# Optimization experiments

Hardware: AMD Instinct MI355X
Metric: run time of the kernel (lower is better)

The kernel has to match this reference:

```python
import jax, jax.numpy as jnp
import numpy as np

EMBED = 1024
HEADS = 16
HEAD_DIM = EMBED // HEADS


def setup_inputs() -> dict:
    key = jax.random.key(0)
    ks = jax.random.split(key, 6)
    N, S = 4, 1024
    query = jax.random.normal(ks[0], (N, S, EMBED), dtype=jnp.float32)
    keys = jax.random.normal(ks[1], (N, S, EMBED), dtype=jnp.float32)
    values = jax.random.normal(ks[2], (N, S, EMBED), dtype=jnp.float32)
    mask = jax.random.randint(ks[3], (N, 1, S, S), 0, 2, dtype=jnp.int32)
    W_out = jax.random.normal(ks[4], (EMBED, EMBED), dtype=jnp.float32) * (1.0 / np.sqrt(EMBED))
    b_out = jax.random.normal(ks[5], (EMBED,), dtype=jnp.float32) * 0.02
    return {"query": query, "keys": keys, "values": values, "mask": mask,
            "W_out": W_out, "b_out": b_out}


def reference(query, keys, values, mask, W_out, b_out):
    N, Q, _ = query.shape
    K = keys.shape[1]
    # NOTE: the torch module never applies its per-head q/k/v Linear layers;
    # only the reshape + attention + fc_out are in the forward path.
    q = query.reshape(N, Q, HEADS, HEAD_DIM)
    k = keys.reshape(N, K, HEADS, HEAD_DIM)
    v = values.reshape(N, K, HEADS, HEAD_DIM)
    # energy: [N, H, Q, K]
    energy = jnp.einsum("bqhd,bkhd->bhqk", q, k)
    energy = jnp.where(mask == 0, jnp.float32(-1e20), energy)
    attn = jax.nn.softmax(energy / jnp.sqrt(jnp.float32(HEAD_DIM)), axis=3)
    out = jnp.einsum("bhqk,bkhd->bqhd", attn, v).reshape(N, Q, HEADS * HEAD_DIM)
    return out @ W_out.T + b_out
```

## Files before the change

### kernel.cpp

```cpp
#include <hip/hip_runtime.h>
#include <math.h>

#define NB 4
#define SL 1024
#define EMB 1024
#define NH 16
#define HD 64
#define QB 64

typedef __attribute__((ext_vector_type(8))) short bf16x8;
typedef __attribute__((ext_vector_type(4))) float f32x4;
typedef __attribute__((ext_vector_type(4))) unsigned u32x4;

static __device__ __forceinline__ unsigned pk2(float a, float b) {
    unsigned x = __float_as_uint(a) + 0x8000u;
    unsigned y = __float_as_uint(b) + 0x8000u;
    return (x >> 16) | (y & 0xFFFF0000u);
}
static __device__ __forceinline__ float exp2_fast(float x) {
    float r; asm("v_exp_f32 %0, %1" : "=v"(r) : "v"(x)); return r;
}
static __device__ __forceinline__ void gload_lds16(const void* g, void* l) {
    __builtin_amdgcn_global_load_lds(
        (const __attribute__((address_space(1))) unsigned int*)g,
        (__attribute__((address_space(3))) unsigned int*)l, 16, 0, 0);
}

#define VMW(n) asm volatile("s_waitcnt vmcnt(" #n ")" ::: "memory")
#define MEMPIN() asm volatile("" ::: "memory")

__global__ __launch_bounds__(256) void prep(
    const float* __restrict__ W, unsigned short* __restrict__ Wb,
    const float* __restrict__ Kf, unsigned short* __restrict__ Kb,
    const float* __restrict__ V, unsigned short* __restrict__ Vt,
    const int* __restrict__ mask, unsigned long long* __restrict__ Mbt)
{
    __shared__ unsigned short sT[128 * 68];
    const int bid = blockIdx.x, tid = threadIdx.x;

    if (bid < 512) {
        int i = (bid * 256 + tid) * 8;
        float4 f0 = *(const float4*)&W[i];
        float4 f1 = *(const float4*)&W[i + 4];
        uint4 u = { pk2(f0.x,f0.y), pk2(f0.z,f0.w), pk2(f1.x,f1.y), pk2(f1.z,f1.w) };
        *(uint4*)&Wb[i] = u;
    } else if (bid < 2560) {
        int t = bid - 512;
        int b = t >> 9, h = (t >> 5) & 15, k0 = (t & 31) * 32;
        int r = tid >> 3, d = (tid & 7) * 8;
        const float* gp = &Kf[((size_t)(b * SL + k0 + r)) * EMB + h * HD + d];
        float4 f0 = *(const float4*)gp, f1 = *(const float4*)(gp + 4);
        uint4 u = { pk2(f0.x,f0.y), pk2(f0.z,f0.w), pk2(f1.x,f1.y), pk2(f1.z,f1.w) };
        *(uint4*)&Kb[((size_t)((b * NH + h) * SL + k0 + r)) * HD + d] = u;
    } else if (bid < 3072) {
        int t = bid - 2560;
        int bh = t >> 3, kb = t & 7;
        int b = bh >> 4, h = bh & 15;
        int k0 = kb * 128;
        #pragma unroll
        for (int i = 0; i < 4; ++i) {
            int lin = (i * 256 + tid) * 8;
            int r = lin >> 6, d = lin & 63;
            const float* gp = &V[((size_t)(b * SL + k0 + r)) * EMB + h * HD + d];
            float4 f0 = *(const float4*)gp, f1 = *(const float4*)(gp + 4);
            uint2 u0 = { pk2(f0.x,f0.y), pk2(f0.z,f0.w) };
            uint2 u1 = { pk2(f1.x,f1.y), pk2(f1.z,f1.w) };
            *(uint2*)&sT[r * 68 + d]     = u0;
            *(uint2*)&sT[r * 68 + d + 4] = u1;
        }
        __syncthreads();
        #pragma unroll
        for (int p = 0; p < 4; ++p) {
            int d = p * 16 + (tid >> 4);
            int c = tid & 15;
            unsigned v[4];
            #pragma unroll
            for (int j = 0; j < 4; ++j) {
                unsigned lo = sT[(c * 8 + 2 * j) * 68 + d];
                unsigned hi = sT[(c * 8 + 2 * j + 1) * 68 + d];
                v[j] = lo | (hi << 16);
            }
            uint4 u = { v[0], v[1], v[2], v[3] };
            *(uint4*)&Vt[((size_t)(bh * HD + d)) * SL + k0 + c * 8] = u;
        }
    } else {
        int t = bid - 3072;
        int lane = tid & 63;
        #pragma unroll
        for (int r = 0; r < 4; ++r) {
            int wid = (t * 4 + (tid >> 6)) * 4 + r;
            int c = wid & 15, q = (wid >> 4) & 1023, bb = wid >> 14;
            int mv = mask[((size_t)bb * SL + q) * SL + c * 64 + lane];
            unsigned long long bits = __ballot(mv != 0);
            if (lane == 0) Mbt[((size_t)bb * 16 + c) * SL + q] = bits;
        }
    }
}

__global__ __launch_bounds__(256, 3) void attn_mfma(
    const float* __restrict__ Q, const unsigned short* __restrict__ Kb,
    const unsigned short* __restrict__ Vt,
    const unsigned long long* __restrict__ Mbt,
    unsigned short* __restrict__ Oa)
{
    const int lin = blockIdx.x;
    const int xcd = lin & 7, slot = lin >> 3;
    const int bh = xcd * 8 + (slot >> 4);
    const int q0 = (slot & 15) * QB;
    const int b = bh >> 4, h = bh & 15;
    const int tid = threadIdx.x;
    const int w = tid >> 6, lane = tid & 63;
    const int m16 = lane & 15, quad = lane >> 4;
    const int lr = lane >> 3, lc = lane & 7;

    __shared__ __align__(16) unsigned short sK[3][64 * 64];
    __shared__ __align__(16) unsigned short sVt[3][64 * 64];

    const size_t vbase = (size_t)(bh * HD) * SL;
    const size_t kbase = (size_t)(bh * SL) * HD;
    const size_t mbase = (size_t)(b * 16) * SL + q0 + w * 16 + m16;

    bf16x8 bQ[2];
    {
        const float* qp = &Q[((size_t)(b * SL + q0 + w * 16 + m16)) * EMB + h * HD + quad * 8];
        float4 f0 = *(const float4*)qp,        f1 = *(const float4*)(qp + 4);
        float4 f2 = *(const float4*)(qp + 32), f3 = *(const float4*)(qp + 36);
        u32x4 u0 = { pk2(f0.x,f0.y), pk2(f0.z,f0.w), pk2(f1.x,f1.y), pk2(f1.z,f1.w) };
        u32x4 u1 = { pk2(f2.x,f2.y), pk2(f2.z,f2.w), pk2(f3.x,f3.y), pk2(f3.z,f3.w) };
        bQ[0] = __builtin_bit_cast(bf16x8, u0);
        bQ[1] = __builtin_bit_cast(bf16x8, u1);
    }
    MEMPIN();
    unsigned long long mbA, mbB, mbC = 0;
    #pragma unroll
    for (int i = 0; i < 2; ++i) {
        int row = w * 16 + i * 8;
        gload_lds16(&Vt[vbase + (size_t)(row + lr) * SL + (lc ^ lr) * 8], &sVt[0][row * 64]);
        gload_lds16(&Kb[kbase + (size_t)(row + lr) * HD + (lc ^ lr) * 8], &sK[0][row * 64]);
    }
    MEMPIN();
    mbA = Mbt[mbase];
    MEMPIN();
    #pragma unroll
    for (int i = 0; i < 2; ++i) {
        int row = w * 16 + i * 8;
        gload_lds16(&Vt[vbase + (size_t)(row + lr) * SL + 64 + (lc ^ lr) * 8], &sVt[1][row * 64]);
        gload_lds16(&Kb[kbase + (size_t)(64 + row + lr) * HD + (lc ^ lr) * 8], &sK[1][row * 64]);
    }
    MEMPIN();
    mbB = Mbt[mbase + SL];
    MEMPIN();

    unsigned short* kc = (unsigned short*)sK[0];
    unsigned short* kn = (unsigned short*)sK[1];
    unsigned short* k2 = (unsigned short*)sK[2];
    unsigned short* vc = (unsigned short*)sVt[0];
    unsigned short* vn = (unsigned short*)sVt[1];
    unsigned short* v2 = (unsigned short*)sVt[2];

    f32x4 O[4] = {};
    f32x4 lacc = {};
    const float CSC = 0.125f * 1.44269504f;
    const short one_bf = (short)0x3F80;
    const bf16x8 ones = { one_bf, one_bf, one_bf, one_bf, one_bf, one_bf, one_bf, one_bf };

    for (int kt = 0; kt < 16; ++kt) {
        if (kt < 15) { VMW(5); } else { VMW(1); }
        __builtin_amdgcn_s_barrier();
        __builtin_amdgcn_sched_barrier(0);

        if (kt < 14) {
            const int k0n = (kt + 2) * 64;
            #pragma unroll
            for (int i = 0; i < 2; ++i) {
                int row = w * 16 + i * 8;
                gload_lds16(&Vt[vbase + (size_t)(row + lr) * SL + k0n + (lc ^ lr) * 8],
                            &v2[row * 64]);
                gload_lds16(&Kb[kbase + (size_t)(k0n + row + lr) * HD + (lc ^ lr) * 8],
                            &k2[row * 64]);
            }
            MEMPIN();
            mbC = Mbt[mbase + (size_t)(kt + 2) * SL];
            MEMPIN();
        }

        f32x4 sc[4];
        __builtin_amdgcn_s_setprio(1);
        #pragma unroll
        for (int t = 0; t < 4; ++t) {
            int krow = t * 16 + m16;
            bf16x8 a0 = *(const bf16x8*)&kc[krow * 64 + ((quad ^ (krow & 7)) * 8)];
            bf16x8 a1 = *(const bf16x8*)&kc[krow * 64 + (((4 + quad) ^ (krow & 7)) * 8)];
            f32x4 z = {0.f, 0.f, 0.f, 0.f};
            sc[t] = __builtin_amdgcn_mfma_f32_16x16x32_bf16(a0, bQ[0], z,     0,0,0);
            sc[t] = __builtin_amdgcn_mfma_f32_16x16x32_bf16(a1, bQ[1], sc[t], 0,0,0);
        }
        __builtin_amdgcn_s_setprio(0);

        bf16x8 bP[2];
        {
            unsigned mlo = (unsigned)mbA, mhi = (unsigned)(mbA >> 32);
            unsigned s0 = mlo >> (quad * 8);
            unsigned s1 = mhi >> (quad * 8);
            unsigned wt[4][2];
            #pragma unroll
            for (int t = 0; t < 4; ++t) {
                wt[t][0] = pk2(exp2_fast(sc[t][0] * CSC), exp2_fast(sc[t][1] * CSC));
                wt[t][1] = pk2(exp2_fast(sc[t][2] * CSC), exp2_fast(sc[t][3] * CSC));
            }
            unsigned g[2][4];
            #pragma unroll
            for (int hh = 0; hh < 2; ++hh)
                #pragma unroll
                for (int p = 0; p < 2; ++p) {
                    unsigned A = wt[2 * hh][p], B = wt[2 * hh + 1][p];
                    asm("v_permlane32_swap_b32 %0, %1" : "+v"(A), "+v"(B));
                    asm("v_permlane16_swap_b32 %0, %1" : "+v"(A), "+v"(B));
                    g[hh][p] = A; g[hh][2 + p] = B;
                }
            #pragma unroll
            for (int hh = 0; hh < 2; ++hh) {
                unsigned sb = hh ? s1 : s0;
                #pragma unroll
                for (int j2 = 0; j2 < 4; ++j2) {
                    unsigned b2 = (sb >> (2 * j2)) & 3u;
                    unsigned am = ((b2 & 1u) ? 0xFFFFu : 0u) | ((b2 & 2u) ? 0xFFFF0000u : 0u);
                    g[hh][j2] &= am;
                }
            }
            u32x4 p0 = { g[0][0], g[0][1], g[0][2], g[0][3] };
            u32x4 p1 = { g[1][0], g[1][1], g[1][2], g[1][3] };
            bP[0] = __builtin_bit_cast(bf16x8, p0);
            bP[1] = __builtin_bit_cast(bf16x8, p1);
        }

        __builtin_amdgcn_s_setprio(1);
        lacc = __builtin_amdgcn_mfma_f32_16x16x32_bf16(ones, bP[0], lacc, 0,0,0);
        lacc = __builtin_amdgcn_mfma_f32_16x16x32_bf16(ones, bP[1], lacc, 0,0,0);

        #pragma unroll
        for (int dt = 0; dt < 4; ++dt) {
            int drow = dt * 16 + m16;
            bf16x8 v0 = *(const bf16x8*)&vc[drow * 64 + ((quad ^ (drow & 7)) * 8)];
            bf16x8 v1 = *(const bf16x8*)&vc[drow * 64 + (((4 + quad) ^ (drow & 7)) * 8)];
            O[dt] = __builtin_amdgcn_mfma_f32_16x16x32_bf16(v0, bP[0], O[dt], 0,0,0);
            O[dt] = __builtin_amdgcn_mfma_f32_16x16x32_bf16(v1, bP[1], O[dt], 0,0,0);
        }
        __builtin_amdgcn_s_setprio(0);

        unsigned short* tk = kc; kc = kn; kn = k2; k2 = tk;
        unsigned short* tv = vc; vc = vn; vn = v2; v2 = tv;
        mbA = mbB; mbB = mbC;
    }

    {
        float inv = 1.f / lacc[0];
        size_t base = ((size_t)(b * SL + q0 + w * 16 + m16)) * EMB + h * HD + quad * 4;
        #pragma unroll
        for (int dt = 0; dt < 4; ++dt) {
            uint2 ow = { pk2(O[dt][0] * inv, O[dt][1] * inv),
                         pk2(O[dt][2] * inv, O[dt][3] * inv) };
            *(uint2*)&Oa[base + dt * 16] = ow;
        }
    }
}

__global__ __launch_bounds__(512, 2) void proj_mfma(
    const unsigned short* __restrict__ A, const unsigned short* __restrict__ Wb,
    const float* __restrict__ bias, float* __restrict__ C)
{
    const int n0 = blockIdx.x * 128;
    const int m0 = blockIdx.y * 128;
    const int tid = threadIdx.x;
    const int w = tid >> 6, lane = tid & 63;
    const int m16 = lane & 15, quad = lane >> 4;
    const int lr = lane >> 3, lc = lane & 7;
    const int wm = (w >> 2) * 64, wn = (w & 3) * 32;

    __shared__ __align__(16) unsigned short sA[2][128 * 64];
    __shared__ __align__(16) unsigned short sW[2][128 * 64];

    f32x4 acc[4][2] = {};

    #pragma unroll
    for (int i = 0; i < 2; ++i) {
        int r = w * 16 + i * 8;
        gload_lds16(&A [(size_t)(m0 + r + lr) * EMB + (lc ^ lr) * 8], &sA[0][r * 64]);
        gload_lds16(&Wb[(size_t)(n0 + r + lr) * EMB + (lc ^ lr) * 8], &sW[0][r * 64]);
    }
    __syncthreads();

    for (int it = 0; it < 16; ++it) {
        const int bf = it & 1;
        if (it < 15) {
            int e0 = (it + 1) * 64;
            #pragma unroll
            for (int i = 0; i < 2; ++i) {
                int r = w * 16 + i * 8;
                gload_lds16(&A [(size_t)(m0 + r + lr) * EMB + e0 + (lc ^ lr) * 8], &sA[bf ^ 1][r * 64]);
                gload_lds16(&Wb[(size_t)(n0 + r + lr) * EMB + e0 + (lc ^ lr) * 8], &sW[bf ^ 1][r * 64]);
            }
        }
        #pragma unroll
        for (int hh = 0; hh < 2; ++hh) {
            bf16x8 af[4], bw[2];
            #pragma unroll
            for (int mt = 0; mt < 4; ++mt) {
                int r = wm + mt * 16 + m16;
                af[mt] = *(const bf16x8*)&sA[bf][r * 64 + (((hh * 4 + quad) ^ (r & 7)) * 8)];
            }
            #pragma unroll
            for (int nt = 0; nt < 2; ++nt) {
                int r = wn + nt * 16 + m16;
                bw[nt] = *(const bf16x8*)&sW[bf][r * 64 + (((hh * 4 + quad) ^ (r & 7)) * 8)];
            }
            #pragma unroll
            for (int mt = 0; mt < 4; ++mt)
                #pragma unroll
                for (int nt = 0; nt < 2; ++nt)
                    acc[mt][nt] = __builtin_amdgcn_mfma_f32_16x16x32_bf16(af[mt], bw[nt], acc[mt][nt], 0,0,0);
        }
        __syncthreads();
    }

    #pragma unroll
    for (int nt = 0; nt < 2; ++nt) {
        float bv = bias[n0 + wn + nt * 16 + m16];
        #pragma unroll
        for (int mt = 0; mt < 4; ++mt) {
            size_t row = (size_t)(m0 + wm + mt * 16 + quad * 4);
            #pragma unroll
            for (int rg = 0; rg < 4; ++rg)
                C[(row + rg) * EMB + n0 + wn + nt * 16 + m16] = acc[mt][nt][rg] + bv;
        }
    }
}

extern "C" void kernel_launch(void* const* d_in, const int* in_sizes, int n_in,
                              void* d_out, int out_size, void* d_ws, size_t ws_size,
                              hipStream_t stream) {
    const float* Q    = (const float*)d_in[0];
    const float* K    = (const float*)d_in[1];
    const float* V    = (const float*)d_in[2];
    const int*   mask = (const int*)  d_in[3];
    const float* W    = (const float*)d_in[4];
    const float* bias = (const float*)d_in[5];

    unsigned short* Oa = (unsigned short*)d_ws;
    unsigned short* Wb = Oa + (size_t)NB * SL * EMB;
    unsigned long long* Mbt = (unsigned long long*)(Wb + (size_t)EMB * EMB);
    unsigned short* Vt = (unsigned short*)(Mbt + (size_t)NB * 16 * SL);
    unsigned short* Kb = Vt + (size_t)NB * NH * HD * SL;

    prep<<<7168, 256, 0, stream>>>(W, Wb, K, Kb, V, Vt, mask, Mbt);
    attn_mfma<<<1024, 256, 0, stream>>>(Q, Kb, Vt, Mbt, Oa);
    proj_mfma<<<dim3(EMB / 128, (NB * SL) / 128), 512, 0, stream>>>(Oa, Wb, bias, (float*)d_out);
}
```

Baseline: 169.6 us.

## Load K and V tiles straight into registers instead of staging through LDS

The attention kernel no longer stages K/Vt tiles through triple-buffered shared memory with async global-to-LDS loads and per-tile barriers. Each wave now loads its MFMA operands directly from global memory into registers, prefetching the next K tile into ping-pong register arrays while V for the current tile is loaded just before use. This removes LDS traffic and the block-wide barriers, but every wave redundantly reads the full K/V tiles from global memory or L2. It also raises register pressure, and the V loads have little latency hiding.

```diff
diff --git a/kernel.cpp b/kernel.cpp
--- a/kernel.cpp
+++ b/kernel.cpp
@@ -26,7 +26,6 @@
         (__attribute__((address_space(3))) unsigned int*)l, 16, 0, 0);
 }
 
-#define VMW(n) asm volatile("s_waitcnt vmcnt(" #n ")" ::: "memory")
 #define MEMPIN() asm volatile("" ::: "memory")
 
 __global__ __launch_bounds__(256) void prep(
@@ -97,6 +96,88 @@
     }
 }
 
+#define TILE(KT, KC, KN)                                                       \
+{                                                                              \
+    const int kt_ = (KT);                                                      \
+    {                                                                          \
+        const unsigned short* vp = Vp + kt_ * 64;                              \
+        _Pragma("unroll")                                                      \
+        for (int dt = 0; dt < 4; ++dt) {                                       \
+            vC[2*dt]   = *(const bf16x8*)&vp[(dt*16 + m16) * SL + quad * 8];   \
+            vC[2*dt+1] = *(const bf16x8*)&vp[(dt*16 + m16) * SL + (4+quad)*8]; \
+        }                                                                      \
+    }                                                                          \
+    MEMPIN();                                                                  \
+    if (kt_ < 15) {                                                            \
+        const unsigned short* kp = Kp + (size_t)(kt_ + 1) * 64 * HD;           \
+        _Pragma("unroll")                                                      \
+        for (int t = 0; t < 4; ++t) {                                          \
+            KN[2*t]   = *(const bf16x8*)&kp[(t*16 + m16) * HD + quad * 8];     \
+            KN[2*t+1] = *(const bf16x8*)&kp[(t*16 + m16) * HD + (4+quad)*8];   \
+        }                                                                      \
+        MEMPIN();                                                              \
+        mbB = Mp[(size_t)(kt_ + 1) * SL];                                      \
+        MEMPIN();                                                              \
+    }                                                                          \
+    __builtin_amdgcn_sched_barrier(0);                                         \
+    f32x4 sc[4];                                                               \
+    __builtin_amdgcn_s_setprio(1);                                             \
+    _Pragma("unroll")                                                          \
+    for (int t = 0; t < 4; ++t) {                                              \
+        f32x4 z = {0.f, 0.f, 0.f, 0.f};                                        \
+        sc[t] = __builtin_amdgcn_mfma_f32_16x16x32_bf16(KC[2*t],   bQ[0], z,     0,0,0); \
+        sc[t] = __builtin_amdgcn_mfma_f32_16x16x32_bf16(KC[2*t+1], bQ[1], sc[t], 0,0,0); \
+    }                                                                          \
+    __builtin_amdgcn_s_setprio(0);                                             \
+    bf16x8 bP[2];                                                              \
+    {                                                                          \
+        unsigned mlo = (unsigned)mbA, mhi = (unsigned)(mbA >> 32);             \
+        unsigned s0 = mlo >> (quad * 8);                                       \
+        unsigned s1 = mhi >> (quad * 8);                                       \
+        unsigned wt[4][2];                                                     \
+        _Pragma("unroll")                                                      \
+        for (int t = 0; t < 4; ++t) {                                          \
+            wt[t][0] = pk2(exp2_fast(sc[t][0] * CSC), exp2_fast(sc[t][1] * CSC)); \
+            wt[t][1] = pk2(exp2_fast(sc[t][2] * CSC), exp2_fast(sc[t][3] * CSC)); \
+        }                                                                      \
+        unsigned g[2][4];                                                      \
+        _Pragma("unroll")                                                      \
+        for (int hh = 0; hh < 2; ++hh) {                                       \
+            _Pragma("unroll")                                                  \
+            for (int p = 0; p < 2; ++p) {                                      \
+                unsigned A = wt[2*hh][p], B = wt[2*hh+1][p];                   \
+                asm("v_permlane32_swap_b32 %0, %1" : "+v"(A), "+v"(B));        \
+                asm("v_permlane16_swap_b32 %0, %1" : "+v"(A), "+v"(B));        \
+                g[hh][p] = A; g[hh][2+p] = B;                                  \
+            }                                                                  \
+        }                                                                      \
+        _Pragma("unroll")                                                      \
+        for (int hh = 0; hh < 2; ++hh) {                                       \
+            unsigned sb = hh ? s1 : s0;                                        \
+            _Pragma("unroll")                                                  \
+            for (int j2 = 0; j2 < 4; ++j2) {                                   \
+                unsigned b2 = (sb >> (2*j2)) & 3u;                             \
+                unsigned am = ((b2 & 1u) ? 0xFFFFu : 0u) | ((b2 & 2u) ? 0xFFFF0000u : 0u); \
+                g[hh][j2] &= am;                                               \
+            }                                                                  \
+        }                                                                      \
+        u32x4 p0 = { g[0][0], g[0][1], g[0][2], g[0][3] };                     \
+        u32x4 p1 = { g[1][0], g[1][1], g[1][2], g[1][3] };                     \
+        bP[0] = __builtin_bit_cast(bf16x8, p0);                                \
+        bP[1] = __builtin_bit_cast(bf16x8, p1);                                \
+    }                                                                          \
+    __builtin_amdgcn_s_setprio(1);                                             \
+    lacc = __builtin_amdgcn_mfma_f32_16x16x32_bf16(ones, bP[0], lacc, 0,0,0);  \
+    lacc = __builtin_amdgcn_mfma_f32_16x16x32_bf16(ones, bP[1], lacc, 0,0,0);  \
+    _Pragma("unroll")                                                          \
+    for (int dt = 0; dt < 4; ++dt) {                                           \
+        O[dt] = __builtin_amdgcn_mfma_f32_16x16x32_bf16(vC[2*dt],   bP[0], O[dt], 0,0,0); \
+        O[dt] = __builtin_amdgcn_mfma_f32_16x16x32_bf16(vC[2*dt+1], bP[1], O[dt], 0,0,0); \
+    }                                                                          \
+    __builtin_amdgcn_s_setprio(0);                                             \
+    mbA = mbB;                                                                 \
+}
+
 __global__ __launch_bounds__(256, 3) void attn_mfma(
     const float* __restrict__ Q, const unsigned short* __restrict__ Kb,
     const unsigned short* __restrict__ Vt,
@@ -111,14 +192,10 @@
     const int tid = threadIdx.x;
     const int w = tid >> 6, lane = tid & 63;
     const int m16 = lane & 15, quad = lane >> 4;
-    const int lr = lane >> 3, lc = lane & 7;
-
-    __shared__ __align__(16) unsigned short sK[3][64 * 64];
-    __shared__ __align__(16) unsigned short sVt[3][64 * 64];
-
-    const size_t vbase = (size_t)(bh * HD) * SL;
-    const size_t kbase = (size_t)(bh * SL) * HD;
-    const size_t mbase = (size_t)(b * 16) * SL + q0 + w * 16 + m16;
+
+    const unsigned short* Kp = Kb + (size_t)bh * SL * HD;
+    const unsigned short* Vp = Vt + (size_t)bh * HD * SL;
+    const unsigned long long* Mp = Mbt + (size_t)(b * 16) * SL + q0 + w * 16 + m16;
 
     bf16x8 bQ[2];
     {
@@ -131,32 +208,16 @@
         bQ[1] = __builtin_bit_cast(bf16x8, u1);
     }
     MEMPIN();
-    unsigned long long mbA, mbB, mbC = 0;
+    bf16x8 kA[8], kB[8], vC[8];
+    unsigned long long mbA, mbB = 0;
     #pragma unroll
-    for (int i = 0; i < 2; ++i) {
-        int row = w * 16 + i * 8;
-        gload_lds16(&Vt[vbase + (size_t)(row + lr) * SL + (lc ^ lr) * 8], &sVt[0][row * 64]);
-        gload_lds16(&Kb[kbase + (size_t)(row + lr) * HD + (lc ^ lr) * 8], &sK[0][row * 64]);
+    for (int t = 0; t < 4; ++t) {
+        kA[2*t]   = *(const bf16x8*)&Kp[(t*16 + m16) * HD + quad * 8];
+        kA[2*t+1] = *(const bf16x8*)&Kp[(t*16 + m16) * HD + (4+quad)*8];
     }
     MEMPIN();
-    mbA = Mbt[mbase];
+    mbA = Mp[0];
     MEMPIN();
-    #pragma unroll
-    for (int i = 0; i < 2; ++i) {
-        int row = w * 16 + i * 8;
-        gload_lds16(&Vt[vbase + (size_t)(row + lr) * SL + 64 + (lc ^ lr) * 8], &sVt[1][row * 64]);
-        gload_lds16(&Kb[kbase + (size_t)(64 + row + lr) * HD + (lc ^ lr) * 8], &sK[1][row * 64]);
-    }
-    MEMPIN();
-    mbB = Mbt[mbase + SL];
-    MEMPIN();
-
-    unsigned short* kc = (unsigned short*)sK[0];
-    unsigned short* kn = (unsigned short*)sK[1];
-    unsigned short* k2 = (unsigned short*)sK[2];
-    unsigned short* vc = (unsigned short*)sVt[0];
-    unsigned short* vn = (unsigned short*)sVt[1];
-    unsigned short* v2 = (unsigned short*)sVt[2];
 
     f32x4 O[4] = {};
     f32x4 lacc = {};
@@ -164,93 +225,9 @@
     const short one_bf = (short)0x3F80;
     const bf16x8 ones = { one_bf, one_bf, one_bf, one_bf, one_bf, one_bf, one_bf, one_bf };
 
-    for (int kt = 0; kt < 16; ++kt) {
-        if (kt < 15) { VMW(5); } else { VMW(1); }
-        __builtin_amdgcn_s_barrier();
-        __builtin_amdgcn_sched_barrier(0);
-
-        if (kt < 14) {
-            const int k0n = (kt + 2) * 64;
-            #pragma unroll
-            for (int i = 0; i < 2; ++i) {
-                int row = w * 16 + i * 8;
-                gload_lds16(&Vt[vbase + (size_t)(row + lr) * SL + k0n + (lc ^ lr) * 8],
-                            &v2[row * 64]);
-                gload_lds16(&Kb[kbase + (size_t)(k0n + row + lr) * HD + (lc ^ lr) * 8],
-                            &k2[row * 64]);
-            }
-            MEMPIN();
-            mbC = Mbt[mbase + (size_t)(kt + 2) * SL];
-            MEMPIN();
-        }
-
-        f32x4 sc[4];
-        __builtin_amdgcn_s_setprio(1);
-        #pragma unroll
-        for (int t = 0; t < 4; ++t) {
-            int krow = t * 16 + m16;
-            bf16x8 a0 = *(const bf16x8*)&kc[krow * 64 + ((quad ^ (krow & 7)) * 8)];
-            bf16x8 a1 = *(const bf16x8*)&kc[krow * 64 + (((4 + quad) ^ (krow & 7)) * 8)];
-            f32x4 z = {0.f, 0.f, 0.f, 0.f};
-            sc[t] = __builtin_amdgcn_mfma_f32_16x16x32_bf16(a0, bQ[0], z,     0,0,0);
-            sc[t] = __builtin_amdgcn_mfma_f32_16x16x32_bf16(a1, bQ[1], sc[t], 0,0,0);
-        }
-        __builtin_amdgcn_s_setprio(0);
-
-        bf16x8 bP[2];
-        {
-            unsigned mlo = (unsigned)mbA, mhi = (unsigned)(mbA >> 32);
-            unsigned s0 = mlo >> (quad * 8);
-            unsigned s1 = mhi >> (quad * 8);
-            unsigned wt[4][2];
-            #pragma unroll
-            for (int t = 0; t < 4; ++t) {
-                wt[t][0] = pk2(exp2_fast(sc[t][0] * CSC), exp2_fast(sc[t][1] * CSC));
-                wt[t][1] = pk2(exp2_fast(sc[t][2] * CSC), exp2_fast(sc[t][3] * CSC));
-            }
-            unsigned g[2][4];
-            #pragma unroll
-            for (int hh = 0; hh < 2; ++hh)
-                #pragma unroll
-                for (int p = 0; p < 2; ++p) {
-                    unsigned A = wt[2 * hh][p], B = wt[2 * hh + 1][p];
-                    asm("v_permlane32_swap_b32 %0, %1" : "+v"(A), "+v"(B));
-                    asm("v_permlane16_swap_b32 %0, %1" : "+v"(A), "+v"(B));
-                    g[hh][p] = A; g[hh][2 + p] = B;
-                }
-            #pragma unroll
-            for (int hh = 0; hh < 2; ++hh) {
-                unsigned sb = hh ? s1 : s0;
-                #pragma unroll
-                for (int j2 = 0; j2 < 4; ++j2) {
-                    unsigned b2 = (sb >> (2 * j2)) & 3u;
-                    unsigned am = ((b2 & 1u) ? 0xFFFFu : 0u) | ((b2 & 2u) ? 0xFFFF0000u : 0u);
-                    g[hh][j2] &= am;
-                }
-            }
-            u32x4 p0 = { g[0][0], g[0][1], g[0][2], g[0][3] };
-            u32x4 p1 = { g[1][0], g[1][1], g[1][2], g[1][3] };
-            bP[0] = __builtin_bit_cast(bf16x8, p0);
-            bP[1] = __builtin_bit_cast(bf16x8, p1);
-        }
-
-        __builtin_amdgcn_s_setprio(1);
-        lacc = __builtin_amdgcn_mfma_f32_16x16x32_bf16(ones, bP[0], lacc, 0,0,0);
-        lacc = __builtin_amdgcn_mfma_f32_16x16x32_bf16(ones, bP[1], lacc, 0,0,0);
-
-        #pragma unroll
-        for (int dt = 0; dt < 4; ++dt) {
-            int drow = dt * 16 + m16;
-            bf16x8 v0 = *(const bf16x8*)&vc[drow * 64 + ((quad ^ (drow & 7)) * 8)];
-            bf16x8 v1 = *(const bf16x8*)&vc[drow * 64 + (((4 + quad) ^ (drow & 7)) * 8)];
-            O[dt] = __builtin_amdgcn_mfma_f32_16x16x32_bf16(v0, bP[0], O[dt], 0,0,0);
-            O[dt] = __builtin_amdgcn_mfma_f32_16x16x32_bf16(v1, bP[1], O[dt], 0,0,0);
-        }
-        __builtin_amdgcn_s_setprio(0);
-
-        unsigned short* tk = kc; kc = kn; kn = k2; k2 = tk;
-        unsigned short* tv = vc; vc = vn; vn = v2; v2 = tv;
-        mbA = mbB; mbB = mbC;
+    for (int i = 0; i < 8; ++i) {
+        TILE(2*i,     kA, kB)
+        TILE(2*i + 1, kB, kA)
     }
 
     {
```

New measurement: 253.7 us. 1.5x slower.

## Double query block per workgroup to 128 rows with 8 waves sharing K/V tiles

Applied to the files above, without the earlier changes.

The attention kernel now handles 128 query rows per workgroup with 512 threads (8 waves), so each K/V tile staged in LDS is reused by twice as many waves. Each wave loads a single 8-row slice of the tile instead of two, which halves per-wave global-to-LDS traffic, and the vmcnt wait is adjusted to match. The Q global loads are also issued before the K/V prefetch so their latency overlaps. In exchange the grid shrinks to 512 blocks and barriers now synchronize 8 waves, which may lower scheduling flexibility or occupancy.

```diff
diff --git a/kernel.cpp b/kernel.cpp
--- a/kernel.cpp
+++ b/kernel.cpp
@@ -6,7 +6,7 @@
 #define EMB 1024
 #define NH 16
 #define HD 64
-#define QB 64
+#define QB 128
 
 typedef __attribute__((ext_vector_type(8))) short bf16x8;
 typedef __attribute__((ext_vector_type(4))) float f32x4;
@@ -97,7 +97,7 @@
     }
 }
 
-__global__ __launch_bounds__(256, 3) void attn_mfma(
+__global__ __launch_bounds__(512, 4) void attn_mfma(
     const float* __restrict__ Q, const unsigned short* __restrict__ Kb,
     const unsigned short* __restrict__ Vt,
     const unsigned long long* __restrict__ Mbt,
@@ -105,51 +105,45 @@
 {
     const int lin = blockIdx.x;
     const int xcd = lin & 7, slot = lin >> 3;
-    const int bh = xcd * 8 + (slot >> 4);
-    const int q0 = (slot & 15) * QB;
+    const int bh = xcd * 8 + (slot >> 3);
+    const int q0 = (slot & 7) * QB;
     const int b = bh >> 4, h = bh & 15;
     const int tid = threadIdx.x;
     const int w = tid >> 6, lane = tid & 63;
     const int m16 = lane & 15, quad = lane >> 4;
     const int lr = lane >> 3, lc = lane & 7;
+    const int srow = w * 8;
 
     __shared__ __align__(16) unsigned short sK[3][64 * 64];
     __shared__ __align__(16) unsigned short sVt[3][64 * 64];
 
     const size_t vbase = (size_t)(bh * HD) * SL;
     const size_t kbase = (size_t)(bh * SL) * HD;
-    const size_t mbase = (size_t)(b * 16) * SL + q0 + w * 16 + m16;
+    const unsigned long long* Mp = Mbt + (size_t)(b * 16) * SL + q0 + w * 16 + m16;
+
+    const float* qp = &Q[((size_t)(b * SL + q0 + w * 16 + m16)) * EMB + h * HD + quad * 8];
+    float4 f0 = *(const float4*)qp,        f1 = *(const float4*)(qp + 4);
+    float4 f2 = *(const float4*)(qp + 32), f3 = *(const float4*)(qp + 36);
+    MEMPIN();
+    unsigned long long mbA, mbB, mbC = 0;
+    gload_lds16(&Vt[vbase + (size_t)(srow + lr) * SL + (lc ^ lr) * 8], &sVt[0][srow * 64]);
+    gload_lds16(&Kb[kbase + (size_t)(srow + lr) * HD + (lc ^ lr) * 8], &sK[0][srow * 64]);
+    MEMPIN();
+    mbA = Mp[0];
+    MEMPIN();
+    gload_lds16(&Vt[vbase + (size_t)(srow + lr) * SL + 64 + (lc ^ lr) * 8], &sVt[1][srow * 64]);
+    gload_lds16(&Kb[kbase + (size_t)(64 + srow + lr) * HD + (lc ^ lr) * 8], &sK[1][srow * 64]);
+    MEMPIN();
+    mbB = Mp[SL];
+    MEMPIN();
 
     bf16x8 bQ[2];
     {
-        const float* qp = &Q[((size_t)(b * SL + q0 + w * 16 + m16)) * EMB + h * HD + quad * 8];
-        float4 f0 = *(const float4*)qp,        f1 = *(const float4*)(qp + 4);
-        float4 f2 = *(const float4*)(qp + 32), f3 = *(const float4*)(qp + 36);
         u32x4 u0 = { pk2(f0.x,f0.y), pk2(f0.z,f0.w), pk2(f1.x,f1.y), pk2(f1.z,f1.w) };
         u32x4 u1 = { pk2(f2.x,f2.y), pk2(f2.z,f2.w), pk2(f3.x,f3.y), pk2(f3.z,f3.w) };
         bQ[0] = __builtin_bit_cast(bf16x8, u0);
         bQ[1] = __builtin_bit_cast(bf16x8, u1);
     }
-    MEMPIN();
-    unsigned long long mbA, mbB, mbC = 0;
-    #pragma unroll
-    for (int i = 0; i < 2; ++i) {
-        int row = w * 16 + i * 8;
-        gload_lds16(&Vt[vbase + (size_t)(row + lr) * SL + (lc ^ lr) * 8], &sVt[0][row * 64]);
-        gload_lds16(&Kb[kbase + (size_t)(row + lr) * HD + (lc ^ lr) * 8], &sK[0][row * 64]);
-    }
-    MEMPIN();
-    mbA = Mbt[mbase];
-    MEMPIN();
-    #pragma unroll
-    for (int i = 0; i < 2; ++i) {
-        int row = w * 16 + i * 8;
-        gload_lds16(&Vt[vbase + (size_t)(row + lr) * SL + 64 + (lc ^ lr) * 8], &sVt[1][row * 64]);
-        gload_lds16(&Kb[kbase + (size_t)(64 + row + lr) * HD + (lc ^ lr) * 8], &sK[1][row * 64]);
-    }
-    MEMPIN();
-    mbB = Mbt[mbase + SL];
-    MEMPIN();
 
     unsigned short* kc = (unsigned short*)sK[0];
     unsigned short* kn = (unsigned short*)sK[1];
@@ -165,22 +159,18 @@
     const bf16x8 ones = { one_bf, one_bf, one_bf, one_bf, one_bf, one_bf, one_bf, one_bf };
 
     for (int kt = 0; kt < 16; ++kt) {
-        if (kt < 15) { VMW(5); } else { VMW(1); }
+        if (kt < 15) { VMW(4); } else { VMW(1); }
         __builtin_amdgcn_s_barrier();
         __builtin_amdgcn_sched_barrier(0);
 
         if (kt < 14) {
             const int k0n = (kt + 2) * 64;
-            #pragma unroll
-            for (int i = 0; i < 2; ++i) {
-                int row = w * 16 + i * 8;
-                gload_lds16(&Vt[vbase + (size_t)(row + lr) * SL + k0n + (lc ^ lr) * 8],
-                            &v2[row * 64]);
-                gload_lds16(&Kb[kbase + (size_t)(k0n + row + lr) * HD + (lc ^ lr) * 8],
-                            &k2[row * 64]);
-            }
+            gload_lds16(&Vt[vbase + (size_t)(srow + lr) * SL + k0n + (lc ^ lr) * 8],
+                        &v2[srow * 64]);
+            gload_lds16(&Kb[kbase + (size_t)(k0n + srow + lr) * HD + (lc ^ lr) * 8],
+                        &k2[srow * 64]);
             MEMPIN();
-            mbC = Mbt[mbase + (size_t)(kt + 2) * SL];
+            mbC = Mp[(size_t)(kt + 2) * SL];
             MEMPIN();
         }
 
@@ -353,6 +343,6 @@
     unsigned short* Kb = Vt + (size_t)NB * NH * HD * SL;
 
     prep<<<7168, 256, 0, stream>>>(W, Wb, K, Kb, V, Vt, mask, Mbt);
-    attn_mfma<<<1024, 256, 0, stream>>>(Q, Kb, Vt, Mbt, Oa);
+    attn_mfma<<<512, 512, 0, stream>>>(Q, Kb, Vt, Mbt, Oa);
     proj_mfma<<<dim3(EMB / 128, (NB * SL) / 128), 512, 0, stream>>>(Oa, Wb, bias, (float*)d_out);
 }
```

Measured after the change: 162.1 us. 1.05x faster.
